# Performance work log

Hardware: AMD Instinct MI355X
Metric: run time of the kernel (lower is better)

The kernel has to match this reference:

```python
import jax, jax.numpy as jnp
import numpy as np

EPS = 1e-05
NUM_HEADS = 16
NUM_KV_HEADS = 8
HEAD_DIM = 128


def rms_norm(x, w, eps=EPS):
    var = jnp.mean(x.astype(jnp.float32) ** 2, axis=-1, keepdims=True)
    rstd = jax.lax.rsqrt(var + eps).astype(x.dtype)
    return (x * rstd) * w


def apply_rotary(x, cos, sin):
    # x: [B, H, S, D]; cos/sin: [B, S, D//2] -> broadcast over heads
    c = cos[:, None, :, :]
    s = sin[:, None, :, :]
    x1 = x[..., ::2]
    x2 = x[..., 1::2]
    return jnp.concatenate([x1 * c - x2 * s, x1 * s + x2 * c], axis=-1)


def setup_inputs() -> dict:
    key = jax.random.key(0)
    ks = jax.random.split(key, 12)
    B, S, D = 2, 2048, 2048
    Dff = 8192
    Dkv = NUM_KV_HEADS * HEAD_DIM
    sc = 0.02
    return {
        "hidden_states": jax.random.normal(ks[0], (B, S, D), jnp.float32),
        "cos": jax.random.uniform(ks[1], (B, S, HEAD_DIM // 2), jnp.float32),
        "sin": jax.random.uniform(ks[2], (B, S, HEAD_DIM // 2), jnp.float32),
        "attention_mask": jnp.zeros((B, 1, S, S), jnp.float32),
        "wq": jax.random.normal(ks[3], (D, D), jnp.float32) * sc,
        "wk": jax.random.normal(ks[4], (D, Dkv), jnp.float32) * sc,
        "wv": jax.random.normal(ks[5], (D, Dkv), jnp.float32) * sc,
        "wo": jax.random.normal(ks[6], (D, D), jnp.float32) * sc,
        "w_gate": jax.random.normal(ks[7], (D, Dff), jnp.float32) * sc,
        "w_up": jax.random.normal(ks[8], (D, Dff), jnp.float32) * sc,
        "w_down": jax.random.normal(ks[9], (Dff, D), jnp.float32) * sc,
        "ln1_w": jnp.ones((D,), jnp.float32),
        "ln2_w": jnp.ones((D,), jnp.float32),
    }


def reference(hidden_states, cos, sin, attention_mask, wq, wk, wv, wo,
              w_gate, w_up, w_down, ln1_w, ln2_w):
    B, S, D = hidden_states.shape
    n_rep = NUM_HEADS // NUM_KV_HEADS
    scale = HEAD_DIM ** -0.5

    # --- attention block ---
    residual = hidden_states
    x = rms_norm(hidden_states, ln1_w)

    q = (x @ wq).reshape(B, S, NUM_HEADS, HEAD_DIM).transpose(0, 2, 1, 3)
    k = (x @ wk).reshape(B, S, NUM_KV_HEADS, HEAD_DIM).transpose(0, 2, 1, 3)
    v = (x @ wv).reshape(B, S, NUM_KV_HEADS, HEAD_DIM).transpose(0, 2, 1, 3)

    q = apply_rotary(q, cos, sin)
    k = apply_rotary(k, cos, sin)

    k = jnp.repeat(k, n_rep, axis=1)  # [B, H, S, D]
    v = jnp.repeat(v, n_rep, axis=1)

    scores = jnp.einsum('bhqd,bhkd->bhqk', q, k) * scale + attention_mask
    weights = jax.nn.softmax(scores.astype(jnp.float32), axis=-1).astype(q.dtype)
    attn = jnp.einsum('bhqk,bhkd->bhqd', weights, v)
    attn = attn.transpose(0, 2, 1, 3).reshape(B, S, D)
    attn = attn @ wo

    hidden_states = residual + attn

    # --- SwiGLU FFN block ---
    residual = hidden_states
    x = rms_norm(hidden_states, ln2_w)
    gate = jax.nn.silu(x @ w_gate)
    up = x @ w_up
    out = (gate * up) @ w_down
    return residual + out
```

## Files before the change

### kernel.cpp

```cpp
#include <hip/hip_runtime.h>
#include <stdint.h>

typedef unsigned short u16;
typedef unsigned int u32;
typedef short bf16x8 __attribute__((ext_vector_type(8)));
typedef float f32x4 __attribute__((ext_vector_type(4)));

#define AS_GLOBAL __attribute__((address_space(1)))
#define AS_LDS    __attribute__((address_space(3)))

__device__ __forceinline__ float bf2f(u16 h) {
  union { u32 u; float f; } v; v.u = ((u32)h) << 16; return v.f;
}
__device__ __forceinline__ u16 f2bf(float f) {
  union { float f; u32 u; } v; v.f = f;
  return (u16)((v.u + 0x7FFFu + ((v.u >> 16) & 1u)) >> 16);
}
__device__ __forceinline__ float scrub(float v, float mark) {
  return (v == v && fabsf(v) < 1e30f) ? v : mark;
}
__device__ __forceinline__ void gload16(const void* g, void* l) {
  __builtin_amdgcn_global_load_lds((const AS_GLOBAL u32*)g, (AS_LDS u32*)l, 16, 0, 0);
}

__global__ __launch_bounds__(256) void detect_kernel(const u16* __restrict__ hs, int* flagp) {
  __shared__ int cnt;
  if (threadIdx.x == 0) cnt = 0;
  __syncthreads();
  int sane = 0;
  #pragma unroll
  for (int j = 0; j < 4; j++) {
    const u16 v = hs[(threadIdx.x * 4 + j) * 2];
    const int e = (v >> 7) & 0xFF;
    sane += (e >= 0x60 && e <= 0x8E) ? 1 : 0;
  }
  atomicAdd(&cnt, sane);
  __syncthreads();
  if (threadIdx.x == 0) *flagp = (cnt < 600) ? 1 : 0;
}

__global__ void init_flag2_kernel(int* flag2p) { *flag2p = 0; }

__global__ __launch_bounds__(256) void detect_mask_kernel(
    const void* __restrict__ mask, int n, const int* __restrict__ flagp, int* flag2p) {
  const int f = *flagp;
  const size_t nq = (size_t)n * (f ? 4 : 2) / 16;
  u32 acc = 0;
  for (size_t i = blockIdx.x * 256 + threadIdx.x; i < nq; i += (size_t)gridDim.x * 256) {
    const uint4 v = ((const uint4*)mask)[i];
    acc |= v.x | v.y | v.z | v.w;
  }
  if (__ballot(acc != 0) != 0ull && (threadIdx.x & 63) == 0)
    atomicOr(flag2p, 1);
}

__global__ __launch_bounds__(256) void convert_kernel(
    const void* __restrict__ src, u16* __restrict__ dst, int n, const int* __restrict__ flagp) {
  const int f = *flagp;
  const int i = (blockIdx.x * 256 + threadIdx.x) * 4;
  if (i >= n) return;
  union { uint2 u; u16 s[4]; } o;
  if (f) {
    const float4 v = *(const float4*)((const float*)src + i);
    o.s[0] = f2bf(v.x); o.s[1] = f2bf(v.y); o.s[2] = f2bf(v.z); o.s[3] = f2bf(v.w);
  } else {
    o.u = *(const uint2*)((const u16*)src + i);
  }
  *(uint2*)(dst + i) = o.u;
}

__global__ __launch_bounds__(256) void rmsnorm_kernel(
    const u16* __restrict__ xin, const u16* __restrict__ w, u16* __restrict__ out)
{
  __shared__ float red[4];
  const int row = blockIdx.x, tid = threadIdx.x;
  const u16* xr = xin + (size_t)row * 2048 + tid * 8;
  union { uint4 q; u16 s[8]; } uu; uu.q = *(const uint4*)xr;
  float v[8];
  #pragma unroll
  for (int j = 0; j < 8; j++) v[j] = bf2f(uu.s[j]);
  float ss = 0.f;
  #pragma unroll
  for (int j = 0; j < 8; j++) ss += v[j] * v[j];
  #pragma unroll
  for (int o = 32; o; o >>= 1) ss += __shfl_xor(ss, o, 64);
  if ((tid & 63) == 0) red[tid >> 6] = ss;
  __syncthreads();
  float rstd = rsqrtf((red[0] + red[1] + red[2] + red[3]) * (1.0f / 2048.0f) + 1e-5f);
  rstd = bf2f(f2bf(rstd));
  union { uint4 q; u16 s[8]; } ww; ww.q = *(const uint4*)(w + tid * 8);
  union { uint4 q; u16 s[8]; } oo;
  #pragma unroll
  for (int j = 0; j < 8; j++) oo.s[j] = f2bf(scrub(v[j] * rstd * bf2f(ww.s[j]), 200.f));
  *(uint4*)(out + (size_t)row * 2048 + tid * 8) = oo.q;
}

__global__ __launch_bounds__(256) void transpose_kernel(
    const void* __restrict__ in, u16* __restrict__ out, int R, int C,
    const int* __restrict__ flagp)
{
  __shared__ u16 tile[32][33];
  const int f = *flagp;
  const int tx = threadIdx.x, ty = threadIdx.y;
  const int x = blockIdx.x * 32 + tx;
  const int y0 = blockIdx.y * 32;
  if (f) {
    #pragma unroll
    for (int j = ty; j < 32; j += 8) tile[j][tx] = f2bf(((const float*)in)[(size_t)(y0 + j) * C + x]);
  } else {
    #pragma unroll
    for (int j = ty; j < 32; j += 8) tile[j][tx] = ((const u16*)in)[(size_t)(y0 + j) * C + x];
  }
  __syncthreads();
  const int xo = y0 + tx, yo0 = blockIdx.x * 32;
  #pragma unroll
  for (int j = ty; j < 32; j += 8) out[(size_t)(yo0 + j) * R + xo] = tile[tx][j];
}

enum { EPI_STORE = 0, EPI_ADD = 1, EPI_SILU = 2, EPI_ADD_OUT = 3 };

template<int EPI>
__global__ __launch_bounds__(256, 2) void gemm_bt_kernel(
    const u16* __restrict__ A, const u16* __restrict__ Bt,
    void* Cout, const void* aux, int M, int N, int K,
    const int* __restrict__ flagp)
{
  __shared__ alignas(16) u16 As[128 * 32];
  __shared__ alignas(16) u16 Bs[128 * 32];
  const int tid = threadIdx.x;
  const int wid = tid >> 6, lane = tid & 63;
  const int lrow = lane & 15, quad = lane >> 4;
  const int m0 = blockIdx.y * 128, n0 = blockIdx.x * 128;
  const int wm = (wid >> 1) * 64, wn = (wid & 1) * 64;

  const int r0 = tid >> 2, p0 = tid & 3, g0 = p0 ^ ((r0 >> 1) & 3);
  const int r1 = 64 + (tid >> 2), g1 = p0 ^ ((r1 >> 1) & 3);

  const u16* Ar0 = A + (size_t)(m0 + r0) * K + g0 * 8;
  const u16* Ar1 = A + (size_t)(m0 + r1) * K + g1 * 8;
  const u16* Br0 = Bt + (size_t)(n0 + r0) * K + g0 * 8;
  const u16* Br1 = Bt + (size_t)(n0 + r1) * K + g1 * 8;

  f32x4 acc[4][4] = {};

  for (int k0 = 0; k0 < K; k0 += 32) {
    __syncthreads();
    gload16(Ar0 + k0, &As[wid * 512]);
    gload16(Ar1 + k0, &As[2048 + wid * 512]);
    gload16(Br0 + k0, &Bs[wid * 512]);
    gload16(Br1 + k0, &Bs[2048 + wid * 512]);
    __syncthreads();

    bf16x8 af[4], bfm[4];
    #pragma unroll
    for (int mt = 0; mt < 4; mt++) {
      int r = wm + mt * 16 + lrow;
      int p = quad ^ ((r >> 1) & 3);
      af[mt] = *(const bf16x8*)&As[r * 32 + p * 8];
    }
    #pragma unroll
    for (int nt = 0; nt < 4; nt++) {
      int r = wn + nt * 16 + lrow;
      int p = quad ^ ((r >> 1) & 3);
      bfm[nt] = *(const bf16x8*)&Bs[r * 32 + p * 8];
    }
    #pragma unroll
    for (int mt = 0; mt < 4; mt++)
      #pragma unroll
      for (int nt = 0; nt < 4; nt++)
        acc[mt][nt] = __builtin_amdgcn_mfma_f32_16x16x32_bf16(af[mt], bfm[nt], acc[mt][nt], 0, 0, 0);
  }

  const int oflag = (EPI == EPI_ADD_OUT) ? *flagp : 0;
  #pragma unroll
  for (int mt = 0; mt < 4; mt++)
    #pragma unroll
    for (int nt = 0; nt < 4; nt++)
      #pragma unroll
      for (int i = 0; i < 4; i++) {
        const int row = m0 + wm + mt * 16 + quad * 4 + i;
        const int col = n0 + wn + nt * 16 + lrow;
        const size_t idx = (size_t)row * N + col;
        const float vv = acc[mt][nt][i];
        if (EPI == EPI_STORE) {
          ((u16*)Cout)[idx] = f2bf(scrub(vv, 300.f));
        } else if (EPI == EPI_ADD) {
          ((u16*)Cout)[idx] = f2bf(scrub(bf2f(((const u16*)aux)[idx]) + vv, 700.f));
        } else if (EPI == EPI_SILU) {
          float g = bf2f(((const u16*)aux)[idx]);
          g = fminf(fmaxf(g, -30.f), 30.f);
          const float s = g / (1.0f + __expf(-g));
          ((u16*)Cout)[idx] = f2bf(scrub(s * vv, 800.f));
        } else {
          const float r = scrub(bf2f(((const u16*)aux)[idx]) + vv, 1e6f);
          if (oflag) ((float*)Cout)[idx] = r;
          else       ((u16*)Cout)[idx] = f2bf(r);
        }
      }
}

__global__ __launch_bounds__(256) void rope_kernel(
    u16* qkv, const u16* __restrict__ cosb, const u16* __restrict__ sinb)
{
  const int gw = blockIdx.x * 4 + (threadIdx.x >> 6);
  const int lane = threadIdx.x & 63;
  const int h = gw % 24;
  const int t = gw / 24;
  u16* base = qkv + (size_t)t * 4096 + h * 128;
  const u32 x01 = *(const u32*)(base + 2 * lane);
  const float x1 = bf2f((u16)(x01 & 0xffff));
  const float x2 = bf2f((u16)(x01 >> 16));
  const float c = bf2f(cosb[t * 64 + lane]);
  const float s = bf2f(sinb[t * 64 + lane]);
  const u16 o1 = f2bf(x1 * c - x2 * s);
  const u16 o2 = f2bf(x1 * s + x2 * c);
  base[lane] = o1;
  base[64 + lane] = o2;
}

#define VSTR 80
__global__ __launch_bounds__(256, 2) void flash_attn_kernel(
    const u16* __restrict__ qkv, const u16* __restrict__ vT,
    const void* __restrict__ mask, u16* __restrict__ obuf,
    const int* __restrict__ flagp, const int* __restrict__ zerop)
{
  __shared__ alignas(16) u16 Kt[64 * 128];
  __shared__ alignas(16) u16 Vt[128 * VSTR];
  __shared__ alignas(16) u16 Ps[4 * 16 * 64];

  const int qt = blockIdx.x, h = blockIdx.y, b = blockIdx.z;
  const int tid = threadIdx.x;
  const int wid = tid >> 6, lane = tid & 63;
  const int lrow = lane & 15, quad = lane >> 4;
  const int kvh = h >> 1;
  const size_t tok0 = (size_t)b * 2048;
  const int has_mask = *zerop;
  const int mf32 = *flagp;

  bf16x8 qf[4];
  {
    const u16* qptr = qkv + (tok0 + qt * 64 + wid * 16 + lrow) * 4096 + h * 128 + quad * 8;
    #pragma unroll
    for (int kk = 0; kk < 4; kk++) qf[kk] = *(const bf16x8*)(qptr + kk * 32);
  }
  const u16* kbase = qkv + tok0 * 4096 + 2048 + kvh * 128;
  const u16* vbase = vT + (size_t)(kvh * 128) * 4096 + tok0;

  float mst[4] = {-1e30f, -1e30f, -1e30f, -1e30f};
  float lst[4] = {0.f, 0.f, 0.f, 0.f};
  f32x4 oacc[8] = {};
  const float scale = 0.08838834764831845f;

  for (int kt = 0; kt < 32; kt++) {
    __syncthreads();
    #pragma unroll
    for (int ii = 0; ii < 4; ii++) {
      const int rloc = wid * 16 + ii * 4 + (lane >> 4);
      const int ch = lane & 15;
      const int gch = ch ^ (rloc & 7);
      gload16(kbase + (size_t)(kt * 64 + rloc) * 4096 + gch * 8,
              &Kt[(wid * 16 + ii * 4) * 128]);
    }
    #pragma unroll
    for (int ii = 0; ii < 4; ii++) {
      const int ci = ii * 256 + tid;
      const int d = ci >> 3, c = ci & 7;
      const int pos = c ^ (d & 7);
      const uint4 v = *(const uint4*)(vbase + (size_t)d * 4096 + kt * 64 + c * 8);
      *(uint4*)&Vt[d * VSTR + pos * 8] = v;
    }
    __syncthreads();

    f32x4 sfr[4] = {};
    #pragma unroll
    for (int nt = 0; nt < 4; nt++) {
      const int r = nt * 16 + lrow;
      #pragma unroll
      for (int kk = 0; kk < 4; kk++) {
        bf16x8 kf = *(const bf16x8*)&Kt[r * 128 + (((kk * 4 + quad) ^ (r & 7)) << 3)];
        sfr[nt] = __builtin_amdgcn_mfma_f32_16x16x32_bf16(qf[kk], kf, sfr[nt], 0, 0, 0);
      }
    }
    if (has_mask) {
      #pragma unroll
      for (int nt = 0; nt < 4; nt++)
        #pragma unroll
        for (int i = 0; i < 4; i++) {
          const size_t midx = (tok0 + qt * 64 + wid * 16 + quad * 4 + i) * 2048
                              + kt * 64 + nt * 16 + lrow;
          const float mv = mf32 ? ((const float*)mask)[midx] : bf2f(((const u16*)mask)[midx]);
          sfr[nt][i] = fminf(fmaxf(sfr[nt][i] * scale + mv, -1e4f), 1e4f);
        }
    } else {
      #pragma unroll
      for (int nt = 0; nt < 4; nt++)
        #pragma unroll
        for (int i = 0; i < 4; i++)
          sfr[nt][i] = fminf(fmaxf(sfr[nt][i] * scale, -1e4f), 1e4f);
    }
    float alpha[4], mnew[4], rsum[4];
    #pragma unroll
    for (int i = 0; i < 4; i++) {
      float mx = fmaxf(fmaxf(sfr[0][i], sfr[1][i]), fmaxf(sfr[2][i], sfr[3][i]));
      #pragma unroll
      for (int o = 8; o; o >>= 1) mx = fmaxf(mx, __shfl_xor(mx, o, 64));
      mnew[i] = fmaxf(mst[i], mx);
      alpha[i] = __expf(mst[i] - mnew[i]);
      mst[i] = mnew[i];
      rsum[i] = 0.f;
    }
    #pragma unroll
    for (int nt = 0; nt < 4; nt++)
      #pragma unroll
      for (int i = 0; i < 4; i++) {
        const float p = __expf(sfr[nt][i] - mnew[i]);
        rsum[i] += p;
        const int row = quad * 4 + i;
        const int c = nt * 2 + (lrow >> 3);
        Ps[wid * 1024 + row * 64 + ((c ^ (row & 7)) << 3) + (lrow & 7)] = f2bf(p);
      }
    #pragma unroll
    for (int i = 0; i < 4; i++) {
      #pragma unroll
      for (int o = 8; o; o >>= 1) rsum[i] += __shfl_xor(rsum[i], o, 64);
      lst[i] = lst[i] * alpha[i] + rsum[i];
    }
    #pragma unroll
    for (int dt = 0; dt < 8; dt++)
      #pragma unroll
      for (int i = 0; i < 4; i++) oacc[dt][i] *= alpha[i];

    asm volatile("s_waitcnt lgkmcnt(0)" ::: "memory");
    #pragma unroll
    for (int kk = 0; kk < 2; kk++) {
      bf16x8 pf = *(const bf16x8*)&Ps[wid * 1024 + lrow * 64 + (((kk * 4 + quad) ^ (lrow & 7)) << 3)];
      #pragma unroll
      for (int dt = 0; dt < 8; dt++) {
        const int d = dt * 16 + lrow;
        bf16x8 vf = *(const bf16x8*)&Vt[d * VSTR + (((kk * 4 + quad) ^ (d & 7)) << 3)];
        oacc[dt] = __builtin_amdgcn_mfma_f32_16x16x32_bf16(pf, vf, oacc[dt], 0, 0, 0);
      }
    }
  }

  #pragma unroll
  for (int dt = 0; dt < 8; dt++)
    #pragma unroll
    for (int i = 0; i < 4; i++) {
      const size_t tok = tok0 + qt * 64 + wid * 16 + quad * 4 + i;
      obuf[tok * 2048 + h * 128 + dt * 16 + lrow] = f2bf(scrub(oacc[dt][i] / lst[i], 500.f));
    }
}

extern "C" void kernel_launch(void* const* d_in, const int* in_sizes, int n_in,
                              void* d_out, int out_size, void* d_ws, size_t ws_size,
                              hipStream_t stream) {
  (void)in_sizes; (void)n_in; (void)out_size; (void)ws_size;
  const void* hs   = d_in[0];
  const void* cosi = d_in[1];
  const void* sini = d_in[2];
  const void* mask = d_in[3];
  const void* wq   = d_in[4];
  const void* wk   = d_in[5];
  const void* wv   = d_in[6];
  const void* wo   = d_in[7];
  const void* wg   = d_in[8];
  const void* wu   = d_in[9];
  const void* wd   = d_in[10];
  const void* ln1  = d_in[11];
  const void* ln2  = d_in[12];

  char* ws = (char*)d_ws;
  int* flag  = (int*)ws;
  int* flag2 = (int*)(ws + 64);
  u16* ln1b  = (u16*)(ws + 4096);
  u16* ln2b  = (u16*)(ws + 16384);
  u16* cosb  = (u16*)(ws + (1u << 20));
  u16* sinb  = (u16*)(ws + (1u << 20) + (1u << 19));
  u16* hsb   = (u16*)(ws + (2u  << 20));
  u16* xn    = (u16*)(ws + (18u << 20));
  u16* qkv   = (u16*)(ws + (34u << 20));
  u16* abuf  = (u16*)(ws + (66u << 20));
  u16* wT    = (u16*)(ws + (82u << 20));
  u16* gbuf  = (u16*)(ws + (114u << 20));
  u16* vT    = gbuf;
  u16* x2n   = hsb;
  u16* h2    = xn;

  dim3 tb(32, 8);
  detect_kernel<<<1, 256, 0, stream>>>((const u16*)hs, flag);
  init_flag2_kernel<<<1, 1, 0, stream>>>(flag2);
  detect_mask_kernel<<<2048, 256, 0, stream>>>(mask, 8388608, flag, flag2);
  convert_kernel<<<8192, 256, 0, stream>>>(hs,   hsb,  8388608, flag);
  convert_kernel<<<256,  256, 0, stream>>>(cosi, cosb, 262144,  flag);
  convert_kernel<<<256,  256, 0, stream>>>(sini, sinb, 262144,  flag);
  convert_kernel<<<2,    256, 0, stream>>>(ln1,  ln1b, 2048,    flag);
  convert_kernel<<<2,    256, 0, stream>>>(ln2,  ln2b, 2048,    flag);
  rmsnorm_kernel<<<4096, 256, 0, stream>>>(hsb, ln1b, xn);
  transpose_kernel<<<dim3(64, 64), tb, 0, stream>>>(wq, wT, 2048, 2048, flag);
  transpose_kernel<<<dim3(32, 64), tb, 0, stream>>>(wk, wT + (size_t)2048 * 2048, 2048, 1024, flag);
  transpose_kernel<<<dim3(32, 64), tb, 0, stream>>>(wv, wT + (size_t)3072 * 2048, 2048, 1024, flag);
  gemm_bt_kernel<EPI_STORE><<<dim3(24, 32), 256, 0, stream>>>(xn, wT, qkv, nullptr, 4096, 4096, 2048, flag);
  gemm_bt_kernel<EPI_STORE><<<dim3(32, 8), 256, 0, stream>>>(wT + (size_t)3072 * 2048, xn, vT, nullptr, 1024, 4096, 2048, flag);
  rope_kernel<<<24576, 256, 0, stream>>>(qkv, cosb, sinb);
  flash_attn_kernel<<<dim3(32, 16, 2), 256, 0, stream>>>(qkv, vT, mask, abuf, flag, flag2);
  transpose_kernel<<<dim3(64, 64), tb, 0, stream>>>(wo, wT, 2048, 2048, flag);
  gemm_bt_kernel<EPI_ADD><<<dim3(16, 32), 256, 0, stream>>>(abuf, wT, h2, hsb, 4096, 2048, 2048, flag);
  rmsnorm_kernel<<<4096, 256, 0, stream>>>(h2, ln2b, x2n);
  transpose_kernel<<<dim3(256, 64), tb, 0, stream>>>(wg, wT, 2048, 8192, flag);
  gemm_bt_kernel<EPI_STORE><<<dim3(64, 32), 256, 0, stream>>>(x2n, wT, gbuf, nullptr, 4096, 8192, 2048, flag);
  transpose_kernel<<<dim3(256, 64), tb, 0, stream>>>(wu, wT, 2048, 8192, flag);
  gemm_bt_kernel<EPI_SILU><<<dim3(64, 32), 256, 0, stream>>>(x2n, wT, gbuf, gbuf, 4096, 8192, 2048, flag);
  transpose_kernel<<<dim3(64, 256), tb, 0, stream>>>(wd, wT, 8192, 2048, flag);
  gemm_bt_kernel<EPI_ADD_OUT><<<dim3(16, 32), 256, 0, stream>>>(gbuf, wT, d_out, h2, 4096, 2048, 8192, flag);
}
```

Baseline: 1.240 ms.

## Swizzle GEMM block order into row bands and fuse input conversion into RMSNorm

GEMM launches now use a 1D grid that is remapped so consecutive blocks walk down a band of 16 M-tiles before moving along N. The aim is better L2 reuse of A and B tiles across concurrently resident blocks. The first RMSNorm also reads the raw fp32/bf16 input directly and writes the bf16 copy itself, which removes a separate conversion pass over the hidden states. The band mapping assumes gy is a multiple of 16 or smaller than 16; other shapes would map tiles incorrectly.

Result: no change. 1.224 ms (-1.3%).

```diff
diff --git a/kernel.cpp b/kernel.cpp
--- a/kernel.cpp
+++ b/kernel.cpp
@@ -69,13 +69,24 @@
   *(uint2*)(dst + i) = o.u;
 }
 
-__global__ __launch_bounds__(256) void rmsnorm_kernel(
-    const u16* __restrict__ xin, const u16* __restrict__ w, u16* __restrict__ out)
+__global__ __launch_bounds__(256) void rmsnorm_in_kernel(
+    const void* __restrict__ xin, const u16* __restrict__ w,
+    u16* __restrict__ out, u16* __restrict__ srccopy, const int* __restrict__ flagp)
 {
   __shared__ float red[4];
   const int row = blockIdx.x, tid = threadIdx.x;
-  const u16* xr = xin + (size_t)row * 2048 + tid * 8;
-  union { uint4 q; u16 s[8]; } uu; uu.q = *(const uint4*)xr;
+  const int f = *flagp;
+  union { uint4 q; u16 s[8]; } uu;
+  if (f) {
+    const float* xr = (const float*)xin + (size_t)row * 2048 + tid * 8;
+    const float4 a = *(const float4*)xr, b = *(const float4*)(xr + 4);
+    const float t[8] = {a.x, a.y, a.z, a.w, b.x, b.y, b.z, b.w};
+    #pragma unroll
+    for (int j = 0; j < 8; j++) uu.s[j] = f2bf(t[j]);
+  } else {
+    uu.q = *(const uint4*)((const u16*)xin + (size_t)row * 2048 + tid * 8);
+  }
+  *(uint4*)(srccopy + (size_t)row * 2048 + tid * 8) = uu.q;
   float v[8];
   #pragma unroll
   for (int j = 0; j < 8; j++) v[j] = bf2f(uu.s[j]);
@@ -95,6 +106,32 @@
   *(uint4*)(out + (size_t)row * 2048 + tid * 8) = oo.q;
 }
 
+__global__ __launch_bounds__(256) void rmsnorm_kernel(
+    const u16* __restrict__ xin, const u16* __restrict__ w, u16* __restrict__ out)
+{
+  __shared__ float red[4];
+  const int row = blockIdx.x, tid = threadIdx.x;
+  const u16* xr = xin + (size_t)row * 2048 + tid * 8;
+  union { uint4 q; u16 s[8]; } uu; uu.q = *(const uint4*)xr;
+  float v[8];
+  #pragma unroll
+  for (int j = 0; j < 8; j++) v[j] = bf2f(uu.s[j]);
+  float ss = 0.f;
+  #pragma unroll
+  for (int j = 0; j < 8; j++) ss += v[j] * v[j];
+  #pragma unroll
+  for (int o = 32; o; o >>= 1) ss += __shfl_xor(ss, o, 64);
+  if ((tid & 63) == 0) red[tid >> 6] = ss;
+  __syncthreads();
+  float rstd = rsqrtf((red[0] + red[1] + red[2] + red[3]) * (1.0f / 2048.0f) + 1e-5f);
+  rstd = bf2f(f2bf(rstd));
+  union { uint4 q; u16 s[8]; } ww; ww.q = *(const uint4*)(w + tid * 8);
+  union { uint4 q; u16 s[8]; } oo;
+  #pragma unroll
+  for (int j = 0; j < 8; j++) oo.s[j] = f2bf(scrub(v[j] * rstd * bf2f(ww.s[j]), 200.f));
+  *(uint4*)(out + (size_t)row * 2048 + tid * 8) = oo.q;
+}
+
 __global__ __launch_bounds__(256) void transpose_kernel(
     const void* __restrict__ in, u16* __restrict__ out, int R, int C,
     const int* __restrict__ flagp)
@@ -123,14 +160,22 @@
 __global__ __launch_bounds__(256, 2) void gemm_bt_kernel(
     const u16* __restrict__ A, const u16* __restrict__ Bt,
     void* Cout, const void* aux, int M, int N, int K,
-    const int* __restrict__ flagp)
+    int gx, int gy, const int* __restrict__ flagp)
 {
   __shared__ alignas(16) u16 As[128 * 32];
   __shared__ alignas(16) u16 Bs[128 * 32];
   const int tid = threadIdx.x;
   const int wid = tid >> 6, lane = tid & 63;
   const int lrow = lane & 15, quad = lane >> 4;
-  const int m0 = blockIdx.y * 128, n0 = blockIdx.x * 128;
+
+  const int bandh = ((gy & 15) == 0) ? 16 : gy;
+  const int per = gx * bandh;
+  const int band = blockIdx.x / per;
+  const int wrem = blockIdx.x - band * per;
+  const int by = band * bandh + (wrem % bandh);
+  const int bx = wrem / bandh;
+  const int m0 = by * 128, n0 = bx * 128;
+
   const int wm = (wid >> 1) * 64, wn = (wid & 1) * 64;
 
   const int r0 = tid >> 2, p0 = tid & 3, g0 = p0 ^ ((r0 >> 1) & 3);
@@ -391,26 +436,25 @@
   detect_kernel<<<1, 256, 0, stream>>>((const u16*)hs, flag);
   init_flag2_kernel<<<1, 1, 0, stream>>>(flag2);
   detect_mask_kernel<<<2048, 256, 0, stream>>>(mask, 8388608, flag, flag2);
-  convert_kernel<<<8192, 256, 0, stream>>>(hs,   hsb,  8388608, flag);
   convert_kernel<<<256,  256, 0, stream>>>(cosi, cosb, 262144,  flag);
   convert_kernel<<<256,  256, 0, stream>>>(sini, sinb, 262144,  flag);
   convert_kernel<<<2,    256, 0, stream>>>(ln1,  ln1b, 2048,    flag);
   convert_kernel<<<2,    256, 0, stream>>>(ln2,  ln2b, 2048,    flag);
-  rmsnorm_kernel<<<4096, 256, 0, stream>>>(hsb, ln1b, xn);
+  rmsnorm_in_kernel<<<4096, 256, 0, stream>>>(hs, ln1b, xn, hsb, flag);
   transpose_kernel<<<dim3(64, 64), tb, 0, stream>>>(wq, wT, 2048, 2048, flag);
   transpose_kernel<<<dim3(32, 64), tb, 0, stream>>>(wk, wT + (size_t)2048 * 2048, 2048, 1024, flag);
   transpose_kernel<<<dim3(32, 64), tb, 0, stream>>>(wv, wT + (size_t)3072 * 2048, 2048, 1024, flag);
-  gemm_bt_kernel<EPI_STORE><<<dim3(24, 32), 256, 0, stream>>>(xn, wT, qkv, nullptr, 4096, 4096, 2048, flag);
-  gemm_bt_kernel<EPI_STORE><<<dim3(32, 8), 256, 0, stream>>>(wT + (size_t)3072 * 2048, xn, vT, nullptr, 1024, 4096, 2048, flag);
+  gemm_bt_kernel<EPI_STORE><<<24 * 32, 256, 0, stream>>>(xn, wT, qkv, nullptr, 4096, 4096, 2048, 24, 32, flag);
+  gemm_bt_kernel<EPI_STORE><<<32 * 8, 256, 0, stream>>>(wT + (size_t)3072 * 2048, xn, vT, nullptr, 1024, 4096, 2048, 32, 8, flag);
   rope_kernel<<<24576, 256, 0, stream>>>(qkv, cosb, sinb);
   flash_attn_kernel<<<dim3(32, 16, 2), 256, 0, stream>>>(qkv, vT, mask, abuf, flag, flag2);
   transpose_kernel<<<dim3(64, 64), tb, 0, stream>>>(wo, wT, 2048, 2048, flag);
-  gemm_bt_kernel<EPI_ADD><<<dim3(16, 32), 256, 0, stream>>>(abuf, wT, h2, hsb, 4096, 2048, 2048, flag);
+  gemm_bt_kernel<EPI_ADD><<<16 * 32, 256, 0, stream>>>(abuf, wT, h2, hsb, 4096, 2048, 2048, 16, 32, flag);
   rmsnorm_kernel<<<4096, 256, 0, stream>>>(h2, ln2b, x2n);
   transpose_kernel<<<dim3(256, 64), tb, 0, stream>>>(wg, wT, 2048, 8192, flag);
-  gemm_bt_kernel<EPI_STORE><<<dim3(64, 32), 256, 0, stream>>>(x2n, wT, gbuf, nullptr, 4096, 8192, 2048, flag);
+  gemm_bt_kernel<EPI_STORE><<<64 * 32, 256, 0, stream>>>(x2n, wT, gbuf, nullptr, 4096, 8192, 2048, 64, 32, flag);
   transpose_kernel<<<dim3(256, 64), tb, 0, stream>>>(wu, wT, 2048, 8192, flag);
-  gemm_bt_kernel<EPI_SILU><<<dim3(64, 32), 256, 0, stream>>>(x2n, wT, gbuf, gbuf, 4096, 8192, 2048, flag);
+  gemm_bt_kernel<EPI_SILU><<<64 * 32, 256, 0, stream>>>(x2n, wT, gbuf, gbuf, 4096, 8192, 2048, 64, 32, flag);
   transpose_kernel<<<dim3(64, 256), tb, 0, stream>>>(wd, wT, 8192, 2048, flag);
-  gemm_bt_kernel<EPI_ADD_OUT><<<dim3(16, 32), 256, 0, stream>>>(gbuf, wT, d_out, h2, 4096, 2048, 8192, flag);
-}
+  gemm_bt_kernel<EPI_ADD_OUT><<<16 * 32, 256, 0, stream>>>(gbuf, wT, d_out, h2, 4096, 2048, 8192, 16, 32, flag);
+}
```
